# Kernel tuning notes

Measured on AMD Instinct MI355X. Metric: run time of the kernel, lower is better.

## Reference

```python
import jax, jax.numpy as jnp
import numpy as np

ABS_DIM, HIDDEN, ACTION_DIM, N_TASKS, B = 512, 512, 18, 16, 8192
W_SCALE = 0.001


def setup_inputs() -> dict:
    key = jax.random.key(0)
    k1, k2, k3, k4, k5 = jax.random.split(key, 5)
    x = jax.random.normal(k1, (B, ABS_DIM), dtype=jnp.float32)
    task_id = jax.random.randint(k2, (B,), 0, N_TASKS)
    action = jax.random.randint(k3, (B,), 0, ACTION_DIM)
    # Per-task weight banks (MultiLinear), w_scale=0.001
    W1 = jax.random.normal(k4, (N_TASKS, ABS_DIM, HIDDEN), dtype=jnp.float32) * W_SCALE
    b1 = jnp.zeros((N_TASKS, HIDDEN), dtype=jnp.float32)
    W2 = jax.random.normal(k5, (N_TASKS, HIDDEN, ACTION_DIM), dtype=jnp.float32) * W_SCALE
    b2 = jnp.zeros((N_TASKS, ACTION_DIM), dtype=jnp.float32)
    return {"x": x, "task_id": task_id, "action": action,
            "W1": W1, "b1": b1, "W2": W2, "b2": b2}


def _multi_linear(x, W, b, task_id):
    # x: [B, din], W: [T, din, dout], b: [T, dout]
    # Compute all experts then select per-sample (dense grouped-GEMM form).
    y_all = jnp.einsum('bi,tio->tbo', x, W) + b[:, None, :]  # [T, B, dout]
    rows = jnp.arange(x.shape[0])
    return y_all[task_id, rows]  # [B, dout]


def reference(x, task_id, action, W1, b1, W2, b2):
    h = jax.nn.relu(_multi_linear(x, W1, b1, task_id))          # [B, H]
    logits = _multi_linear(h, W2, b2, task_id)                  # [B, A]
    logprobs = jax.nn.log_softmax(logits, axis=1)               # [B, A]
    rows = jnp.arange(x.shape[0])
    log_pi_a = logprobs[rows, action][:, None]                  # [B, 1]
    ent = -jnp.sum(jnp.exp(logprobs) * logprobs, axis=1, keepdims=True)  # [B, 1]
    # forward output: concat of log_pi_a and entropy (action passes through)
    return jnp.concatenate([log_pi_a, ent], axis=1)             # [B, 2]
```

## Files before the change

kernel.cpp:

```cpp
#include <hip/hip_runtime.h>
#include <hip/hip_bf16.h>

#define B_N   8192
#define DIN   512
#define DH    512
#define NACT  18
#define NTASK 16
#define BM    64
#define GBN   128
#define BK    64
#define PJ    20
#define NSLOT 640

typedef __attribute__((ext_vector_type(8))) short  short8v;
typedef __attribute__((ext_vector_type(8))) unsigned short ushort8v;
typedef __attribute__((ext_vector_type(4))) float  float4v;
typedef __attribute__((ext_vector_type(2))) float  float2v;

typedef const __attribute__((address_space(1))) void* gas_ptr;
typedef __attribute__((address_space(3))) void* las_ptr;

__device__ __forceinline__ unsigned short f2bf(float f) {
  union { float f; unsigned int u; } c; c.f = f;
  unsigned int u = c.u;
  u += 0x7fffu + ((u >> 16) & 1u);
  return (unsigned short)(u >> 16);
}

__global__ __launch_bounds__(256) void k_prep(
    const float* __restrict__ W1, const float* __restrict__ W2,
    const int* __restrict__ task_id,
    short* __restrict__ W1T, short* __restrict__ W2T,
    int* __restrict__ tbl, int* __restrict__ rowidx) {
  __shared__ __align__(16) short ldsA[64][72];
  __shared__ float ldsB[64 * 19];
  __shared__ int s_cnt[NTASK], s_cur[NTASK];
  int bx = blockIdx.x, tid = threadIdx.x;

  if (bx == 0) {
    if (tid < NTASK) s_cnt[tid] = 0;
    __syncthreads();
    for (int i = tid; i < B_N; i += 256) atomicAdd(&s_cnt[task_id[i]], 1);
    __syncthreads();
    if (tid == 0) {
      int acc = 0;
#pragma unroll
      for (int t = 0; t < NTASK; ++t) {
        int c = s_cnt[t];
        tbl[t] = c; tbl[16 + t] = acc; s_cur[t] = acc;
        acc += c;
      }
    }
    __syncthreads();
    for (int i = tid; i < B_N; i += 256) {
      int t = task_id[i];
      rowidx[atomicAdd(&s_cur[t], 1)] = i;
    }
  } else if (bx <= 1024) {
    int r = bx & 7;
    int q = ((bx - r) >> 3) - (r == 0 ? 1 : 0);
    int t = r + ((q >> 6) << 3);
    int sub = q & 63;
    int kb = sub >> 3, nb = sub & 7;
    int kr = tid >> 2, c16 = (tid & 3) << 4;
    const float* src = W1 + ((size_t)t * DIN + (size_t)(kb * 64 + kr)) * DH + nb * 64 + c16;
#pragma unroll
    for (int p = 0; p < 4; ++p) {
      float4v v = *(const float4v*)(src + p * 4);
#pragma unroll
      for (int i = 0; i < 4; ++i) ldsA[c16 + p * 4 + i][kr] = (short)f2bf(v[i]);
    }
    __syncthreads();
    int n = tid >> 2, k16 = (tid & 3) << 4;
    short* dst = W1T + ((size_t)t * DH + nb * 64 + n) * DIN + kb * 64 + k16;
    *(ushort8v*)dst       = *(ushort8v*)&ldsA[n][k16];
    *(ushort8v*)(dst + 8) = *(ushort8v*)&ldsA[n][k16 + 8];
  } else {
    int u = bx - 1025;
    int t = u >> 3, k0 = (u & 7) * 64;
    for (int i = tid; i < 64 * NACT; i += 256) {
      int kk = i / NACT, j = i - kk * NACT;
      ldsB[kk * 19 + j] = W2[((size_t)t * DIN + k0 + kk) * NACT + j];
    }
    __syncthreads();
    for (int o = tid; o < 32 * 64; o += 256) {
      int j = o >> 6, kk = o & 63;
      float val = (j < NACT) ? ldsB[kk * 19 + j] : 0.0f;
      W2T[((size_t)t * 32 + j) * DIN + k0 + kk] = (short)f2bf(val);
    }
  }
}

__global__ __launch_bounds__(256, 3) void k_gemm1(
    const float* __restrict__ x, const float* __restrict__ bias1,
    const short* __restrict__ W1T, const short* __restrict__ W2Tg,
    const int* __restrict__ tbl, const int* __restrict__ rowidx,
    float* __restrict__ pbuf) {
  __shared__ __align__(16) short sA[2][BM * 72];
  __shared__ __align__(16) short sB[2][GBN * BK];
  short* sH  = sB[0];
  short* sW2 = sB[1];
  __shared__ int s_rows[64];
  int tid = threadIdx.x, lane = tid & 63, wave = tid >> 6;

  int b = blockIdx.x;
  int t = -1, rel = 0;
  if (b < NSLOT) {
    int r = b & 7, q = b >> 3;
    int n0t = (tbl[r] + 63) >> 6, n1t = (tbl[r + 8] + 63) >> 6;
    if (q < 4 * n0t) { t = r; rel = q; }
    else if (q < 4 * (n0t + n1t)) { t = r + 8; rel = q - 4 * n0t; }
    else return;
  } else {
    int j = b - NSLOT;
    for (int r = 0; r < 8; ++r) {
      int n0t = (tbl[r] + 63) >> 6, n1t = (tbl[r + 8] + 63) >> 6;
      int P = 4 * (n0t + n1t);
      int S = (P > 80) ? (P - 80) : 0;
      if (j < S) {
        int q = 80 + j;
        if (q < 4 * n0t) { t = r; rel = q; }
        else { t = r + 8; rel = q - 4 * n0t; }
        break;
      }
      j -= S;
    }
    if (t < 0) return;
  }
  int itile = rel >> 2, cs = rel & 3;
  int cnt_t = tbl[t], off_t = tbl[16 + t];
  int row0 = off_t + itile * 64;
  int mcnt = cnt_t - itile * 64; if (mcnt > 64) mcnt = 64;
  int n0 = cs * GBN;
  int wm = wave >> 1, wn = wave & 1;

  if (tid < 64) {
    int idx = row0 + tid;
    if (idx > B_N - 1) idx = B_N - 1;
    s_rows[tid] = rowidx[idx];
  }
  __syncthreads();

  int arow = tid >> 2, akc = (tid & 3) << 4;
  const float* xrow = x + (size_t)s_rows[arow] * DIN + akc;
  const short* Bbase = W1T + ((size_t)t * DH + n0) * DIN;

#define STAGE_B(buf, k0e)                                                    \
  _Pragma("unroll") for (int it = 0; it < 4; ++it) {                         \
    int ch = it * 256 + tid; int row = ch >> 3, cc = ch & 7;                 \
    int sc = cc ^ (row & 7);                                                 \
    __builtin_amdgcn_global_load_lds(                                        \
        (gas_ptr)(const void*)(Bbase + (size_t)row * DIN + (k0e) + sc * 8),  \
        (las_ptr)(void*)(&sB[buf][ch * 8]), 16, 0, 0);                       \
  }
#define STAGE_A(buf, k0e) {                                                  \
    const float* xs_ = xrow + (k0e);                                         \
    float4v v0 = *(const float4v*)xs_;                                       \
    float4v v1 = *(const float4v*)(xs_ + 4);                                 \
    float4v v2 = *(const float4v*)(xs_ + 8);                                 \
    float4v v3 = *(const float4v*)(xs_ + 12);                                \
    ushort8v p0, p1;                                                         \
    _Pragma("unroll") for (int i_ = 0; i_ < 4; ++i_) {                       \
      p0[i_] = f2bf(v0[i_]); p0[4 + i_] = f2bf(v1[i_]);                      \
      p1[i_] = f2bf(v2[i_]); p1[4 + i_] = f2bf(v3[i_]); }                    \
    *(ushort8v*)&sA[buf][arow * 72 + akc] = p0;                              \
    *(ushort8v*)&sA[buf][arow * 72 + akc + 8] = p1; }

  STAGE_B(0, 0)
  STAGE_A(0, 0)
  asm volatile("s_waitcnt vmcnt(0)" ::: "memory");
  __syncthreads();

  float4v acc[2][4];
#pragma unroll
  for (int i = 0; i < 2; ++i)
#pragma unroll
    for (int j = 0; j < 4; ++j) acc[i][j] = (float4v)0.0f;

  for (int step = 0; step < 8; ++step) {
    int p = step & 1;
    if (step < 7) {
      STAGE_B(p ^ 1, (step + 1) * BK)
      STAGE_A(p ^ 1, (step + 1) * BK)
    }
#pragma unroll
    for (int ks = 0; ks < 2; ++ks) {
      short8v a[2], bfr[4];
#pragma unroll
      for (int fm = 0; fm < 2; ++fm) {
        int r = wm * 32 + fm * 16 + (lane & 15);
        int c = ks * 4 + (lane >> 4);
        a[fm] = *(const short8v*)&sA[p][r * 72 + c * 8];
      }
#pragma unroll
      for (int fn = 0; fn < 4; ++fn) {
        int r = wn * 64 + fn * 16 + (lane & 15);
        int c = (ks * 4 + (lane >> 4)) ^ (r & 7);
        bfr[fn] = *(const short8v*)&sB[p][r * BK + c * 8];
      }
#pragma unroll
      for (int fm = 0; fm < 2; ++fm)
#pragma unroll
        for (int fn = 0; fn < 4; ++fn)
          acc[fm][fn] = __builtin_amdgcn_mfma_f32_16x16x32_bf16(a[fm], bfr[fn], acc[fm][fn], 0, 0, 0);
    }
    asm volatile("s_waitcnt vmcnt(0)" ::: "memory");
    __syncthreads();
  }

  float bias[4];
#pragma unroll
  for (int fn = 0; fn < 4; ++fn)
    bias[fn] = bias1[t * DH + n0 + wn * 64 + fn * 16 + (lane & 15)];
#pragma unroll
  for (int fn = 0; fn < 4; ++fn) {
    int n = wn * 64 + fn * 16 + (lane & 15);
#pragma unroll
    for (int fm = 0; fm < 2; ++fm) {
#pragma unroll
      for (int r = 0; r < 4; ++r) {
        int m = wm * 32 + fm * 16 + ((lane >> 4) << 2) + r;
        float v = fmaxf(acc[fm][fn][r] + bias[fn], 0.0f);
        *(short*)((char*)sH + m * 256 + (((n >> 3) ^ (m & 7)) << 4) + ((n & 7) << 1)) =
            (short)f2bf(v);
      }
    }
  }
#pragma unroll
  for (int it = 0; it < 2; ++it) {
    int ch = it * 256 + tid;
    int j = ch >> 4, c2 = ch & 15;
    ushort8v w = *(const ushort8v*)(W2Tg + ((size_t)t * 32 + j) * DIN + n0 + c2 * 8);
    *(ushort8v*)&sW2[(j * 16 + (c2 ^ (j & 7))) * 8] = w;
  }
  __syncthreads();

  float4v acc2[2];
  acc2[0] = (float4v)0.0f; acc2[1] = (float4v)0.0f;
#pragma unroll
  for (int ks = 0; ks < 4; ++ks) {
    int mrow = wave * 16 + (lane & 15);
    int ca = (ks * 4 + (lane >> 4)) ^ (mrow & 7);
    short8v af = *(const short8v*)((char*)sH + mrow * 256 + (ca << 4));
#pragma unroll
    for (int fn = 0; fn < 2; ++fn) {
      int j = fn * 16 + (lane & 15);
      int cb = (ks * 4 + (lane >> 4)) ^ (j & 7);
      short8v bf = *(const short8v*)&sW2[(j * 16 + cb) * 8];
      acc2[fn] = __builtin_amdgcn_mfma_f32_16x16x32_bf16(af, bf, acc2[fn], 0, 0, 0);
    }
  }
#pragma unroll
  for (int fn = 0; fn < 2; ++fn) {
#pragma unroll
    for (int r = 0; r < 4; ++r) {
      int m = wave * 16 + ((lane >> 4) << 2) + r;
      int j = fn * 16 + (lane & 15);
      if (m < mcnt && j < PJ)
        pbuf[((size_t)cs * B_N + row0 + m) * PJ + j] = acc2[fn][r];
    }
  }
#undef STAGE_B
#undef STAGE_A
}

__global__ __launch_bounds__(256) void k_soft(
    const float* __restrict__ pbuf, const float* __restrict__ bias2,
    const int* __restrict__ task_id, const int* __restrict__ action,
    const int* __restrict__ rowidx, float* __restrict__ out) {
  __shared__ float acc[256 * PJ];
  int tid = threadIdx.x;
  int base = blockIdx.x * 256;
#pragma unroll
  for (int it = 0; it < 5; ++it) {
    int idx = it * 256 + tid;
    int row = idx / 5, j4 = idx - row * 5;
    float4v s = (float4v)0.0f;
#pragma unroll
    for (int c = 0; c < 4; ++c)
      s += *(const float4v*)&pbuf[((size_t)c * B_N + base + row) * PJ + j4 * 4];
    *(float4v*)&acc[row * PJ + j4 * 4] = s;
  }
  __syncthreads();

  int srow = base + tid;
  int orig = rowidx[srow];
  int t = task_id[orig], act = action[orig];
  float lg[NACT];
#pragma unroll
  for (int j = 0; j < NACT; ++j) lg[j] = acc[tid * PJ + j] + bias2[t * NACT + j];
  float mx = lg[0];
#pragma unroll
  for (int j = 1; j < NACT; ++j) mx = fmaxf(mx, lg[j]);
  float s1 = 0.0f, s2 = 0.0f, la = 0.0f;
#pragma unroll
  for (int j = 0; j < NACT; ++j) {
    float e = __expf(lg[j] - mx);
    s1 += e; s2 += e * lg[j];
    la = (j == act) ? lg[j] : la;
  }
  float logZ = __logf(s1);
  float2v o;
  o[0] = la - mx - logZ;
  o[1] = (mx + logZ) - s2 / s1;
  *(float2v*)(out + (size_t)orig * 2) = o;
}

extern "C" void kernel_launch(void* const* d_in, const int* in_sizes, int n_in,
                              void* d_out, int out_size, void* d_ws, size_t ws_size,
                              hipStream_t stream) {
  const float* x       = (const float*)d_in[0];
  const int*   task_id = (const int*)d_in[1];
  const int*   action  = (const int*)d_in[2];
  const float* W1      = (const float*)d_in[3];
  const float* b1      = (const float*)d_in[4];
  const float* W2      = (const float*)d_in[5];
  const float* b2      = (const float*)d_in[6];
  float* out = (float*)d_out;

  char* ws = (char*)d_ws;
  int* tbl    = (int*)ws;
  int* rowidx = (int*)(ws + 4096);
  size_t off = 36864;
  short* W1T  = (short*)(ws + off);  off += (size_t)NTASK * DH * DIN * 2;
  short* W2T  = (short*)(ws + off);  off += (size_t)NTASK * 32 * DIN * 2;
  float* pbuf = (float*)(ws + off);

  k_prep<<<1153, 256, 0, stream>>>(W1, W2, task_id, W1T, W2T, tbl, rowidx);
  k_gemm1<<<NSLOT + 576, 256, 0, stream>>>(x, b1, W1T, W2T, tbl, rowidx, pbuf);
  k_soft<<<32, 256, 0, stream>>>(pbuf, b2, task_id, action, rowidx, out);
}
```

Baseline: 43.07 us.

## Pre-convert x to bf16 in prep kernel and stage A via async LDS loads

Adds 1024 blocks to the prep kernel that convert x from fp32 to bf16 into a workspace buffer. The GEMM kernel then stages A tiles with global_load_lds using an XOR-swizzled layout instead of fp32 register loads, per-element conversion and LDS stores. The main k-loop is also fully unrolled. This halves A-operand bytes in the GEMM and frees VALU work from the inner loop. The cost is an extra 8 MB of write plus read traffic for the bf16 copy of x in the prep pass.

```diff
diff --git a/kernel.cpp b/kernel.cpp
--- a/kernel.cpp
+++ b/kernel.cpp
@@ -29,8 +29,8 @@
 
 __global__ __launch_bounds__(256) void k_prep(
     const float* __restrict__ W1, const float* __restrict__ W2,
-    const int* __restrict__ task_id,
-    short* __restrict__ W1T, short* __restrict__ W2T,
+    const float* __restrict__ x, const int* __restrict__ task_id,
+    short* __restrict__ W1T, short* __restrict__ W2T, short* __restrict__ xs,
     int* __restrict__ tbl, int* __restrict__ rowidx) {
   __shared__ __align__(16) short ldsA[64][72];
   __shared__ float ldsB[64 * 19];
@@ -75,7 +75,7 @@
     short* dst = W1T + ((size_t)t * DH + nb * 64 + n) * DIN + kb * 64 + k16;
     *(ushort8v*)dst       = *(ushort8v*)&ldsA[n][k16];
     *(ushort8v*)(dst + 8) = *(ushort8v*)&ldsA[n][k16 + 8];
-  } else {
+  } else if (bx <= 1152) {
     int u = bx - 1025;
     int t = u >> 3, k0 = (u & 7) * 64;
     for (int i = tid; i < 64 * NACT; i += 256) {
@@ -88,15 +88,33 @@
       float val = (j < NACT) ? ldsB[kk * 19 + j] : 0.0f;
       W2T[((size_t)t * 32 + j) * DIN + k0 + kk] = (short)f2bf(val);
     }
+  } else {
+    int u = bx - 1153;
+    int row = u * 8 + (tid >> 5);
+    int c16 = (tid & 31) * 16;
+    const float* src = x + (size_t)row * DIN + c16;
+    float4v v0 = *(const float4v*)(src);
+    float4v v1 = *(const float4v*)(src + 4);
+    float4v v2 = *(const float4v*)(src + 8);
+    float4v v3 = *(const float4v*)(src + 12);
+    ushort8v p0, p1;
+#pragma unroll
+    for (int i = 0; i < 4; ++i) {
+      p0[i] = f2bf(v0[i]); p0[4 + i] = f2bf(v1[i]);
+      p1[i] = f2bf(v2[i]); p1[4 + i] = f2bf(v3[i]);
+    }
+    short* dst = xs + (size_t)row * DIN + c16;
+    *(ushort8v*)dst       = p0;
+    *(ushort8v*)(dst + 8) = p1;
   }
 }
 
 __global__ __launch_bounds__(256, 3) void k_gemm1(
-    const float* __restrict__ x, const float* __restrict__ bias1,
+    const short* __restrict__ xs, const float* __restrict__ bias1,
     const short* __restrict__ W1T, const short* __restrict__ W2Tg,
     const int* __restrict__ tbl, const int* __restrict__ rowidx,
     float* __restrict__ pbuf) {
-  __shared__ __align__(16) short sA[2][BM * 72];
+  __shared__ __align__(16) short sA[2][BM * BK];
   __shared__ __align__(16) short sB[2][GBN * BK];
   short* sH  = sB[0];
   short* sW2 = sB[1];
@@ -141,10 +159,19 @@
   }
   __syncthreads();
 
-  int arow = tid >> 2, akc = (tid & 3) << 4;
-  const float* xrow = x + (size_t)s_rows[arow] * DIN + akc;
+  int r0 = tid >> 3, acc_ = tid & 7;
+  int asc = acc_ ^ (r0 & 7);
+  const short* a0 = xs + (size_t)s_rows[r0]      * DIN + asc * 8;
+  const short* a1 = xs + (size_t)s_rows[r0 + 32] * DIN + asc * 8;
   const short* Bbase = W1T + ((size_t)t * DH + n0) * DIN;
 
+#define STAGE_A(buf, k0e) {                                                  \
+    __builtin_amdgcn_global_load_lds(                                        \
+        (gas_ptr)(const void*)(a0 + (k0e)),                                  \
+        (las_ptr)(void*)(&sA[buf][tid * 8]), 16, 0, 0);                      \
+    __builtin_amdgcn_global_load_lds(                                        \
+        (gas_ptr)(const void*)(a1 + (k0e)),                                  \
+        (las_ptr)(void*)(&sA[buf][(256 + tid) * 8]), 16, 0, 0); }
 #define STAGE_B(buf, k0e)                                                    \
   _Pragma("unroll") for (int it = 0; it < 4; ++it) {                         \
     int ch = it * 256 + tid; int row = ch >> 3, cc = ch & 7;                 \
@@ -153,21 +180,9 @@
         (gas_ptr)(const void*)(Bbase + (size_t)row * DIN + (k0e) + sc * 8),  \
         (las_ptr)(void*)(&sB[buf][ch * 8]), 16, 0, 0);                       \
   }
-#define STAGE_A(buf, k0e) {                                                  \
-    const float* xs_ = xrow + (k0e);                                         \
-    float4v v0 = *(const float4v*)xs_;                                       \
-    float4v v1 = *(const float4v*)(xs_ + 4);                                 \
-    float4v v2 = *(const float4v*)(xs_ + 8);                                 \
-    float4v v3 = *(const float4v*)(xs_ + 12);                                \
-    ushort8v p0, p1;                                                         \
-    _Pragma("unroll") for (int i_ = 0; i_ < 4; ++i_) {                       \
-      p0[i_] = f2bf(v0[i_]); p0[4 + i_] = f2bf(v1[i_]);                      \
-      p1[i_] = f2bf(v2[i_]); p1[4 + i_] = f2bf(v3[i_]); }                    \
-    *(ushort8v*)&sA[buf][arow * 72 + akc] = p0;                              \
-    *(ushort8v*)&sA[buf][arow * 72 + akc + 8] = p1; }
-
+
+  STAGE_A(0, 0)
   STAGE_B(0, 0)
-  STAGE_A(0, 0)
   asm volatile("s_waitcnt vmcnt(0)" ::: "memory");
   __syncthreads();
 
@@ -177,11 +192,12 @@
 #pragma unroll
     for (int j = 0; j < 4; ++j) acc[i][j] = (float4v)0.0f;
 
+#pragma unroll
   for (int step = 0; step < 8; ++step) {
-    int p = step & 1;
+    const int p = step & 1;
     if (step < 7) {
+      STAGE_A(p ^ 1, (step + 1) * BK)
       STAGE_B(p ^ 1, (step + 1) * BK)
-      STAGE_A(p ^ 1, (step + 1) * BK)
     }
 #pragma unroll
     for (int ks = 0; ks < 2; ++ks) {
@@ -189,8 +205,8 @@
 #pragma unroll
       for (int fm = 0; fm < 2; ++fm) {
         int r = wm * 32 + fm * 16 + (lane & 15);
-        int c = ks * 4 + (lane >> 4);
-        a[fm] = *(const short8v*)&sA[p][r * 72 + c * 8];
+        int c = (ks * 4 + (lane >> 4)) ^ (r & 7);
+        a[fm] = *(const short8v*)&sA[p][r * BK + c * 8];
       }
 #pragma unroll
       for (int fn = 0; fn < 4; ++fn) {
@@ -324,9 +340,10 @@
   size_t off = 36864;
   short* W1T  = (short*)(ws + off);  off += (size_t)NTASK * DH * DIN * 2;
   short* W2T  = (short*)(ws + off);  off += (size_t)NTASK * 32 * DIN * 2;
+  short* xs   = (short*)(ws + off);  off += (size_t)B_N * DIN * 2;
   float* pbuf = (float*)(ws + off);
 
-  k_prep<<<1153, 256, 0, stream>>>(W1, W2, task_id, W1T, W2T, tbl, rowidx);
-  k_gemm1<<<NSLOT + 576, 256, 0, stream>>>(x, b1, W1T, W2T, tbl, rowidx, pbuf);
+  k_prep<<<2177, 256, 0, stream>>>(W1, W2, x, task_id, W1T, W2T, xs, tbl, rowidx);
+  k_gemm1<<<NSLOT + 576, 256, 0, stream>>>(xs, b1, W1T, W2T, tbl, rowidx, pbuf);
   k_soft<<<32, 256, 0, stream>>>(pbuf, b2, task_id, action, rowidx, out);
 }
```

Result: faster. 42.06 us (-2.3%).
